# Kernel tuning notes

Measured on AMD Instinct MI355X. Metric: run time of the kernel, lower is better.

Reference implementation:

```python
import jax, jax.numpy as jnp
import numpy as np

N_NODES = 10000
N_EDGES = 640000
D_IN, D_HID, D_OUT = 128, 256, 64


def setup_inputs() -> dict:
    key = jax.random.key(0)
    k = jax.random.split(key, 8)
    h = jax.random.normal(k[0], (N_NODES, D_IN), dtype=jnp.float32)
    w = jax.random.uniform(k[1], (N_EDGES, 1), dtype=jnp.float32)
    src = jax.random.randint(k[2], (N_EDGES,), 0, N_NODES, dtype=jnp.int32)
    dst = jax.random.randint(k[3], (N_EDGES,), 0, N_NODES, dtype=jnp.int32)
    W1 = jax.random.normal(k[4], (2 * D_IN, D_HID), dtype=jnp.float32) * (1.0 / np.sqrt(2 * D_IN))
    b1 = jnp.zeros((D_HID,), dtype=jnp.float32)
    W2 = jax.random.normal(k[5], (2 * D_HID, D_OUT), dtype=jnp.float32) * (1.0 / np.sqrt(2 * D_HID))
    b2 = jnp.zeros((D_OUT,), dtype=jnp.float32)
    return {"h": h, "w": w, "src": src, "dst": dst, "W1": W1, "b1": b1, "W2": W2, "b2": b2}


def _sage_layer(h, w, src, dst, W, b, n_nodes):
    # message: m_e = h[src_e] * w_e  (scalar edge weight broadcast over features)
    m = h[src] * w  # [E, D]
    # mean scatter-reduce over incoming edges per destination node
    s = jax.ops.segment_sum(m, dst, num_segments=n_nodes)          # [N, D]
    deg = jax.ops.segment_sum(jnp.ones((dst.shape[0],), h.dtype), dst, num_segments=n_nodes)
    h_N = jnp.where(deg[:, None] > 0, s / jnp.maximum(deg, 1.0)[:, None], 0.0)
    # concat + linear
    return jnp.concatenate([h, h_N], axis=1) @ W + b


def reference(h, w, src, dst, W1, b1, W2, b2):
    n = h.shape[0]
    x = _sage_layer(h, w, src, dst, W1, b1, n)
    x = jax.nn.relu(x)
    return _sage_layer(x, w, src, dst, W2, b2, n)
```

## Files before the change

kernel.cpp:

```cpp
#include <hip/hip_runtime.h>
#include <hip/hip_fp16.h>


#define NSUB 4
#define CAPS 64
#define FB 2048

typedef _Float16 f16x8 __attribute__((ext_vector_type(8)));
typedef float f32x4 __attribute__((ext_vector_type(4)));

#define ACC8(q, wt)                                              \
  {                                                              \
    const float2 t0 = __half22float2(*(const __half2*)&(q).x);   \
    const float2 t1 = __half22float2(*(const __half2*)&(q).y);   \
    const float2 t2 = __half22float2(*(const __half2*)&(q).z);   \
    const float2 t3 = __half22float2(*(const __half2*)&(q).w);   \
    a[0] += t0.x * (wt); a[1] += t0.y * (wt);                    \
    a[2] += t1.x * (wt); a[3] += t1.y * (wt);                    \
    a[4] += t2.x * (wt); a[5] += t2.y * (wt);                    \
    a[6] += t3.x * (wt); a[7] += t3.y * (wt);                    \
  }


__global__ __launch_bounds__(256) void fill_k(const int* __restrict__ src,
                                              const int* __restrict__ dst,
                                              const float* __restrict__ w,
                                              const float* __restrict__ h,
                                              const float* __restrict__ W1,
                                              const float* __restrict__ W2,
                                              int* __restrict__ cursor,
                                              unsigned int* __restrict__ ebuf,
                                              __half* __restrict__ hh,
                                              __half* __restrict__ W1z,
                                              __half* __restrict__ W2z,
                                              int E, int N, int NH4) {
  if (blockIdx.x < FB) {
    const int grp = blockIdx.x & 7;
    const int bi = blockIdx.x >> 3;
    const int nbg = FB >> 3;
    const int chunk = (N + 7) >> 3;
    const int lo = grp * chunk;
    const int hi = min(N, lo + chunk);
    for (int i = bi * 256 + threadIdx.x; i < E; i += nbg * 256) {
      const int d = dst[i];
      if (d >= lo && d < hi) {
        const int sub = i & (NSUB - 1);
        const int p = atomicAdd(&cursor[d * NSUB + sub], 1);
        if (p < CAPS) {
          const __half hw = __float2half_rn(w[i]);
          ebuf[((size_t)(d * NSUB + sub)) * CAPS + p] =
              ((unsigned int)src[i] << 16) | (unsigned int)__half_as_ushort(hw);
        }
      }
    }
    return;
  }
  const int t = (blockIdx.x - FB) * 256 + threadIdx.x;
  if (t < NH4) {
    const float4 v = reinterpret_cast<const float4*>(h)[t];
    reinterpret_cast<__half2*>(hh)[2 * t] = __floats2half2_rn(v.x, v.y);
    reinterpret_cast<__half2*>(hh)[2 * t + 1] = __floats2half2_rn(v.z, v.w);
    return;
  }
  const int tw1 = t - NH4;
  if (tw1 < 8192) {
    const int ln = tw1 & 63;
    const int nt = (tw1 >> 6) & 15;
    const int kc = tw1 >> 10;
    const int kbase = kc * 32 + (ln >> 4) * 8;
    const int n = nt * 16 + (ln & 15);
    __half tmp[8];
#pragma unroll
    for (int j = 0; j < 8; ++j)
      tmp[j] = __float2half_rn(W1[(size_t)(kbase + j) * 256 + n]);
    *reinterpret_cast<uint4*>(W1z + (size_t)tw1 * 8) = *reinterpret_cast<uint4*>(tmp);
    return;
  }
  const int tw2 = tw1 - 8192;
  if (tw2 < 4096) {
    const int ln = tw2 & 63;
    const int nt = (tw2 >> 6) & 7;
    const int kc = tw2 >> 9;
    const int kbase = kc * 32 + (ln >> 4) * 8;
    const int np = nt * 16 + (ln & 15);
    __half tmp[8];
#pragma unroll
    for (int j = 0; j < 8; ++j) {
      const int k = kbase + j;
      const float v = (np < 64) ? W2[(size_t)k * 64 + np]
                                : W2[(size_t)(256 + k) * 64 + (np - 64)];
      tmp[j] = __float2half_rn(v);
    }
    *reinterpret_cast<uint4*>(W2z + (size_t)tw2 * 8) = *reinterpret_cast<uint4*>(tmp);
  }
}


__global__ __launch_bounds__(256) void ag1g_k(const __half* __restrict__ hh,
                                              const unsigned int* __restrict__ ebuf,
                                              const int* __restrict__ cnt,
                                              const __half* __restrict__ W1z,
                                              const float* __restrict__ b1,
                                              const __half* __restrict__ W2z,
                                              __half* __restrict__ Z,
                                              float* __restrict__ U, int N) {
  const int chunk = (N + 7) >> 3;
  const int g8 = blockIdx.x & 7;
  const int kb = blockIdx.x >> 3;
  const int locbase = kb * 16;
  const int nbase = g8 * chunk + locbase;
  const int tid = threadIdx.x;
  const int wv = tid >> 6;
  const int lane = tid & 63;
  const int g = lane >> 4;
  const int f = lane & 15;

  __shared__ alignas(16) __half As[16][136];
  __shared__ alignas(16) __half Hs[16][264];
  __shared__ alignas(16) float S[16][132];

  const uint4* __restrict__ H = reinterpret_cast<const uint4*>(hh);

#pragma unroll
  for (int i = 0; i < 4; ++i) {
    const int row = wv * 4 + i;
    const int loc = locbase + row;
    const int n = g8 * chunk + loc;
    const bool valid = (loc < chunk) && (n < N);
    int m[NSUB] = {0, 0, 0, 0};
    unsigned int pk[NSUB] = {0u, 0u, 0u, 0u};
    if (valid) {
      const int4 c4 = *reinterpret_cast<const int4*>(cnt + n * NSUB);
      m[0] = min(c4.x, CAPS);
      m[1] = min(c4.y, CAPS);
      m[2] = min(c4.z, CAPS);
      m[3] = min(c4.w, CAPS);
      const unsigned int* __restrict__ bkt = ebuf + ((size_t)(n * NSUB)) * CAPS;
#pragma unroll
      for (int s = 0; s < NSUB; ++s)
        pk[s] = (lane < m[s]) ? bkt[s * CAPS + lane] : 0u;
    }
    const int deg = m[0] + m[1] + m[2] + m[3];
    const int mMax = max(max(m[0], m[1]), max(m[2], m[3]));

    float a[8] = {};
    for (int j = 0; j < mMax; j += 4) {
      unsigned int p[NSUB];
#pragma unroll
      for (int s = 0; s < NSUB; ++s) p[s] = __shfl(pk[s], j + g);
      uint4 q[NSUB];
#pragma unroll
      for (int s = 0; s < NSUB; ++s) q[s] = H[(size_t)(p[s] >> 16) * 16 + f];
#pragma unroll
      for (int s = 0; s < NSUB; ++s) {
        const float wt = __half2float(__ushort_as_half((unsigned short)p[s]));
        ACC8(q[s], wt)
      }
    }
#pragma unroll
    for (int r = 0; r < 8; ++r) {
      a[r] += __shfl_xor(a[r], 16);
      a[r] += __shfl_xor(a[r], 32);
    }
    if (lane < 16) {
      const float inv = (deg > 0) ? 1.0f / (float)deg : 0.0f;
      __half tmp[8];
#pragma unroll
      for (int r = 0; r < 8; ++r) tmp[r] = __float2half_rn(a[r] * inv);
      *reinterpret_cast<uint4*>(&As[row][f * 8]) = *reinterpret_cast<uint4*>(tmp);
    }
  }
  __syncthreads();

  const int w = wv;
  const int row_in = nbase + (lane & 15);
  const int qoff = (lane >> 4) * 8;
  const int colq = lane & 15;
  const int rowq = (lane >> 4) * 4;

  f32x4 acc[4] = {};
  const __half* __restrict__ Ah = hh + (size_t)row_in * 128;
#pragma unroll
  for (int kc = 0; kc < 8; ++kc) {
    const __half* asrc =
        (kc < 4) ? (Ah + kc * 32 + qoff) : (&As[lane & 15][(kc - 4) * 32 + qoff]);
    const f16x8 af = *reinterpret_cast<const f16x8*>(asrc);
    const __half* bbase = W1z + ((size_t)(kc * 16 + w * 4) * 64 + lane) * 8;
#pragma unroll
    for (int nt = 0; nt < 4; ++nt) {
      const f16x8 bf = *reinterpret_cast<const f16x8*>(bbase + (size_t)nt * 64 * 8);
      acc[nt] = __builtin_amdgcn_mfma_f32_16x16x32_f16(af, bf, acc[nt], 0, 0, 0);
    }
  }
#pragma unroll
  for (int nt = 0; nt < 4; ++nt) {
    const int col = w * 64 + nt * 16 + colq;
    const float bz = b1[col];
#pragma unroll
    for (int r = 0; r < 4; ++r)
      Hs[rowq + r][col] = __float2half_rn(fmaxf(acc[nt][r] + bz, 0.f));
  }
  __syncthreads();

  f32x4 accz[2] = {};
#pragma unroll
  for (int kc = 0; kc < 8; ++kc) {
    const f16x8 af = *reinterpret_cast<const f16x8*>(&Hs[lane & 15][kc * 32 + qoff]);
    const __half* bbase = W2z + ((size_t)(kc * 8 + w * 2) * 64 + lane) * 8;
#pragma unroll
    for (int nt = 0; nt < 2; ++nt) {
      const f16x8 bf = *reinterpret_cast<const f16x8*>(bbase + (size_t)nt * 64 * 8);
      accz[nt] = __builtin_amdgcn_mfma_f32_16x16x32_f16(af, bf, accz[nt], 0, 0, 0);
    }
  }
#pragma unroll
  for (int nt = 0; nt < 2; ++nt) {
    const int col = w * 32 + nt * 16 + colq;
#pragma unroll
    for (int r = 0; r < 4; ++r) S[rowq + r][col] = accz[nt][r];
  }
  __syncthreads();
  {
    const int row = tid >> 4, c4 = tid & 15;
    if (locbase + row < chunk && nbase + row < N) {
      const float4 v = make_float4(S[row][c4 * 4], S[row][c4 * 4 + 1],
                                   S[row][c4 * 4 + 2], S[row][c4 * 4 + 3]);
      *reinterpret_cast<float4*>(&U[(size_t)(nbase + row) * 64 + c4 * 4]) = v;
    }
  }
  if (tid < 128) {
    const int row = tid >> 3, c8 = tid & 7;
    if (locbase + row < chunk && nbase + row < N) {
      const float* s = &S[row][64 + c8 * 8];
      const __half2 h0 = __floats2half2_rn(s[0], s[1]);
      const __half2 h1 = __floats2half2_rn(s[2], s[3]);
      const __half2 h2 = __floats2half2_rn(s[4], s[5]);
      const __half2 h3 = __floats2half2_rn(s[6], s[7]);
      uint4 q;
      q.x = *reinterpret_cast<const unsigned int*>(&h0);
      q.y = *reinterpret_cast<const unsigned int*>(&h1);
      q.z = *reinterpret_cast<const unsigned int*>(&h2);
      q.w = *reinterpret_cast<const unsigned int*>(&h3);
      *reinterpret_cast<uint4*>(&Z[(size_t)(nbase + row) * 64 + c8 * 8]) = q;
    }
  }
}


__global__ __launch_bounds__(256) void agg2z_k(const __half* __restrict__ Z,
                                               const float* __restrict__ U,
                                               const float* __restrict__ b2,
                                               const unsigned int* __restrict__ ebuf,
                                               const int* __restrict__ cnt,
                                               float* __restrict__ out, int N) {
  const int chunk = (N + 7) >> 3;
  const int g8 = blockIdx.x & 7;
  const int k = blockIdx.x >> 3;
  const int loc = k * 4 + (threadIdx.x >> 6);
  const int n = g8 * chunk + loc;
  if (loc >= chunk || n >= N) return;
  const int lane = threadIdx.x & 63;
  const int g = lane >> 3;
  const int f = lane & 7;
  const uint4* __restrict__ Zr = reinterpret_cast<const uint4*>(Z);

  const int4 c4 = *reinterpret_cast<const int4*>(cnt + n * NSUB);
  int m[NSUB];
  m[0] = min(c4.x, CAPS);
  m[1] = min(c4.y, CAPS);
  m[2] = min(c4.z, CAPS);
  m[3] = min(c4.w, CAPS);
  const int deg = m[0] + m[1] + m[2] + m[3];
  const int mMax = max(max(m[0], m[1]), max(m[2], m[3]));

  const unsigned int* __restrict__ bkt = ebuf + ((size_t)(n * NSUB)) * CAPS;
  unsigned int pk[NSUB];
#pragma unroll
  for (int s = 0; s < NSUB; ++s)
    pk[s] = (lane < m[s]) ? bkt[s * CAPS + lane] : 0u;

  float a[8] = {};
  for (int j = 0; j < mMax; j += 16) {
    unsigned int pA[NSUB], pB[NSUB];
#pragma unroll
    for (int s = 0; s < NSUB; ++s) {
      pA[s] = __shfl(pk[s], j + g);
      pB[s] = __shfl(pk[s], j + 8 + g);
    }
    uint4 qA[NSUB], qB[NSUB];
#pragma unroll
    for (int s = 0; s < NSUB; ++s) {
      qA[s] = Zr[(size_t)(pA[s] >> 16) * 8 + f];
      qB[s] = Zr[(size_t)(pB[s] >> 16) * 8 + f];
    }
#pragma unroll
    for (int s = 0; s < NSUB; ++s) {
      const float wA = __half2float(__ushort_as_half((unsigned short)pA[s]));
      const float wB = __half2float(__ushort_as_half((unsigned short)pB[s]));
      ACC8(qA[s], wA)
      ACC8(qB[s], wB)
    }
  }
#pragma unroll
  for (int r = 0; r < 8; ++r) {
    a[r] += __shfl_xor(a[r], 8);
    a[r] += __shfl_xor(a[r], 16);
    a[r] += __shfl_xor(a[r], 32);
  }
  if (lane < 8) {
    const float inv = (deg > 0) ? 1.0f / (float)deg : 0.0f;
    const float4 u0 = *reinterpret_cast<const float4*>(&U[(size_t)n * 64 + f * 8]);
    const float4 u1 = *reinterpret_cast<const float4*>(&U[(size_t)n * 64 + f * 8 + 4]);
    const float4 z0 = *reinterpret_cast<const float4*>(&b2[f * 8]);
    const float4 z1 = *reinterpret_cast<const float4*>(&b2[f * 8 + 4]);
    float4 o0, o1;
    o0.x = a[0] * inv + u0.x + z0.x;
    o0.y = a[1] * inv + u0.y + z0.y;
    o0.z = a[2] * inv + u0.z + z0.z;
    o0.w = a[3] * inv + u0.w + z0.w;
    o1.x = a[4] * inv + u1.x + z1.x;
    o1.y = a[5] * inv + u1.y + z1.y;
    o1.z = a[6] * inv + u1.z + z1.z;
    o1.w = a[7] * inv + u1.w + z1.w;
    *reinterpret_cast<float4*>(&out[(size_t)n * 64 + f * 8]) = o0;
    *reinterpret_cast<float4*>(&out[(size_t)n * 64 + f * 8 + 4]) = o1;
  }
}


extern "C" void kernel_launch(void* const* d_in, const int* in_sizes, int n_in,
                              void* d_out, int out_size, void* d_ws, size_t ws_size,
                              hipStream_t stream) {
  const float* h   = (const float*)d_in[0];
  const float* w   = (const float*)d_in[1];
  const int*   src = (const int*)d_in[2];
  const int*   dst = (const int*)d_in[3];
  const float* W1  = (const float*)d_in[4];
  const float* b1  = (const float*)d_in[5];
  const float* W2  = (const float*)d_in[6];
  const float* b2  = (const float*)d_in[7];
  float* out = (float*)d_out;

  const int N = in_sizes[0] / 128;
  const int E = in_sizes[2];

  char* ws = (char*)d_ws;
  size_t o = 0;
  auto alloc = [&](size_t bytes) -> void* {
    void* p = ws + o;
    o = (o + bytes + 255) & ~(size_t)255;
    return p;
  };
  int*          cursor = (int*)alloc((size_t)N * NSUB * 4);
  unsigned int* ebuf   = (unsigned int*)alloc((size_t)N * NSUB * CAPS * 4);
  __half*       hh     = (__half*)alloc((size_t)N * 128 * 2);
  __half*       Z      = (__half*)alloc((size_t)N * 64 * 2);
  float*        U      = (float*)alloc((size_t)N * 64 * 4);
  __half*       W1z    = (__half*)alloc((size_t)256 * 256 * 2);
  __half*       W2z    = (__half*)alloc((size_t)256 * 128 * 2);

  const int NH4 = N * 32;
  const int prep_blocks = (NH4 + 8192 + 4096 + 255) / 256;
  const int chunk = (N + 7) >> 3;

  hipMemsetAsync(cursor, 0, (size_t)N * NSUB * 4, stream);
  fill_k<<<FB + prep_blocks, 256, 0, stream>>>(src, dst, w, h, W1, W2, cursor,
                                               ebuf, hh, W1z, W2z, E, N, NH4);
  ag1g_k<<<8 * ((chunk + 15) >> 4), 256, 0, stream>>>(hh, ebuf, cursor, W1z, b1,
                                                      W2z, Z, U, N);
  agg2z_k<<<8 * ((chunk + 3) / 4), 256, 0, stream>>>(Z, U, b2, ebuf, cursor, out, N);
}
```

Before: 137.9 us.

## Interleave edge buckets and overlap four-row gathers in fused SAGE layer

Edge buckets are now stored interleaved by sub-bucket, so each lane loads its four packed entries with a single 16-byte load instead of four strided loads. The layer-1 aggregation processes a wave's four destination rows in one interleaved loop, which gives more independent gathers in flight and better latency hiding. It also prefetches the self-feature MFMA operands, biases and the layer-2 residual inputs ahead of the gather loop. The cost is higher register pressure from four accumulator sets, which may reduce occupancy.

```diff
diff --git a/kernel.cpp b/kernel.cpp
--- a/kernel.cpp
+++ b/kernel.cpp
@@ -9,16 +9,16 @@
 typedef _Float16 f16x8 __attribute__((ext_vector_type(8)));
 typedef float f32x4 __attribute__((ext_vector_type(4)));
 
-#define ACC8(q, wt)                                              \
+#define ACC8P(acc, q, wt)                                        \
   {                                                              \
     const float2 t0 = __half22float2(*(const __half2*)&(q).x);   \
     const float2 t1 = __half22float2(*(const __half2*)&(q).y);   \
     const float2 t2 = __half22float2(*(const __half2*)&(q).z);   \
     const float2 t3 = __half22float2(*(const __half2*)&(q).w);   \
-    a[0] += t0.x * (wt); a[1] += t0.y * (wt);                    \
-    a[2] += t1.x * (wt); a[3] += t1.y * (wt);                    \
-    a[4] += t2.x * (wt); a[5] += t2.y * (wt);                    \
-    a[6] += t3.x * (wt); a[7] += t3.y * (wt);                    \
+    (acc)[0] += t0.x * (wt); (acc)[1] += t0.y * (wt);            \
+    (acc)[2] += t1.x * (wt); (acc)[3] += t1.y * (wt);            \
+    (acc)[4] += t2.x * (wt); (acc)[5] += t2.y * (wt);            \
+    (acc)[6] += t3.x * (wt); (acc)[7] += t3.y * (wt);            \
   }
 
 
@@ -48,7 +48,7 @@
         const int p = atomicAdd(&cursor[d * NSUB + sub], 1);
         if (p < CAPS) {
           const __half hw = __float2half_rn(w[i]);
-          ebuf[((size_t)(d * NSUB + sub)) * CAPS + p] =
+          ebuf[((size_t)d * CAPS + p) * NSUB + sub] =
               ((unsigned int)src[i] << 16) | (unsigned int)__half_as_ushort(hw);
         }
       }
@@ -121,70 +121,91 @@
 
   const uint4* __restrict__ H = reinterpret_cast<const uint4*>(hh);
 
-#pragma unroll
-  for (int i = 0; i < 4; ++i) {
-    const int row = wv * 4 + i;
-    const int loc = locbase + row;
-    const int n = g8 * chunk + loc;
-    const bool valid = (loc < chunk) && (n < N);
-    int m[NSUB] = {0, 0, 0, 0};
-    unsigned int pk[NSUB] = {0u, 0u, 0u, 0u};
-    if (valid) {
-      const int4 c4 = *reinterpret_cast<const int4*>(cnt + n * NSUB);
-      m[0] = min(c4.x, CAPS);
-      m[1] = min(c4.y, CAPS);
-      m[2] = min(c4.z, CAPS);
-      m[3] = min(c4.w, CAPS);
-      const unsigned int* __restrict__ bkt = ebuf + ((size_t)(n * NSUB)) * CAPS;
-#pragma unroll
-      for (int s = 0; s < NSUB; ++s)
-        pk[s] = (lane < m[s]) ? bkt[s * CAPS + lane] : 0u;
-    }
-    const int deg = m[0] + m[1] + m[2] + m[3];
-    const int mMax = max(max(m[0], m[1]), max(m[2], m[3]));
-
-    float a[8] = {};
-    for (int j = 0; j < mMax; j += 4) {
-      unsigned int p[NSUB];
-#pragma unroll
-      for (int s = 0; s < NSUB; ++s) p[s] = __shfl(pk[s], j + g);
-      uint4 q[NSUB];
-#pragma unroll
-      for (int s = 0; s < NSUB; ++s) q[s] = H[(size_t)(p[s] >> 16) * 16 + f];
-#pragma unroll
-      for (int s = 0; s < NSUB; ++s) {
-        const float wt = __half2float(__ushort_as_half((unsigned short)p[s]));
-        ACC8(q[s], wt)
-      }
-    }
-#pragma unroll
-    for (int r = 0; r < 8; ++r) {
-      a[r] += __shfl_xor(a[r], 16);
-      a[r] += __shfl_xor(a[r], 32);
-    }
-    if (lane < 16) {
-      const float inv = (deg > 0) ? 1.0f / (float)deg : 0.0f;
-      __half tmp[8];
-#pragma unroll
-      for (int r = 0; r < 8; ++r) tmp[r] = __float2half_rn(a[r] * inv);
-      *reinterpret_cast<uint4*>(&As[row][f * 8]) = *reinterpret_cast<uint4*>(tmp);
-    }
-  }
-  __syncthreads();
-
-  const int w = wv;
   const int row_in = nbase + (lane & 15);
   const int qoff = (lane >> 4) * 8;
   const int colq = lane & 15;
   const int rowq = (lane >> 4) * 4;
-
+  const __half* __restrict__ Ah = hh + (size_t)row_in * 128;
+  f16x8 afp[4];
+#pragma unroll
+  for (int kc = 0; kc < 4; ++kc)
+    afp[kc] = *reinterpret_cast<const f16x8*>(Ah + kc * 32 + qoff);
+  float bz[4];
+#pragma unroll
+  for (int nt = 0; nt < 4; ++nt) bz[nt] = b1[wv * 64 + nt * 16 + colq];
+
+  int mM[4], degv[4];
+  unsigned int pk[4][NSUB];
+  float a[4][8];
+#pragma unroll
+  for (int i = 0; i < 4; ++i) {
+#pragma unroll
+    for (int r = 0; r < 8; ++r) a[i][r] = 0.f;
+    const int loc = locbase + wv * 4 + i;
+    const int n = g8 * chunk + loc;
+    const bool valid = (loc < chunk) && (n < N);
+    int m0 = 0, m1 = 0, m2 = 0, m3 = 0;
+    uint4 pkv = make_uint4(0u, 0u, 0u, 0u);
+    if (valid) {
+      const int4 c4 = *reinterpret_cast<const int4*>(cnt + n * NSUB);
+      m0 = min(c4.x, CAPS);
+      m1 = min(c4.y, CAPS);
+      m2 = min(c4.z, CAPS);
+      m3 = min(c4.w, CAPS);
+      pkv = *reinterpret_cast<const uint4*>(ebuf + ((size_t)n * CAPS + lane) * NSUB);
+    }
+    pk[i][0] = (lane < m0) ? pkv.x : 0u;
+    pk[i][1] = (lane < m1) ? pkv.y : 0u;
+    pk[i][2] = (lane < m2) ? pkv.z : 0u;
+    pk[i][3] = (lane < m3) ? pkv.w : 0u;
+    degv[i] = m0 + m1 + m2 + m3;
+    mM[i] = max(max(m0, m1), max(m2, m3));
+  }
+  const int maxAll = max(max(mM[0], mM[1]), max(mM[2], mM[3]));
+
+  for (int j = 0; j < maxAll; j += 4) {
+#pragma unroll
+    for (int i = 0; i < 4; ++i) {
+      if (j < mM[i]) {
+        unsigned int p[NSUB];
+#pragma unroll
+        for (int s = 0; s < NSUB; ++s) p[s] = __shfl(pk[i][s], j + g);
+        uint4 q[NSUB];
+#pragma unroll
+        for (int s = 0; s < NSUB; ++s) q[s] = H[(size_t)(p[s] >> 16) * 16 + f];
+#pragma unroll
+        for (int s = 0; s < NSUB; ++s) {
+          const float wt = __half2float(__ushort_as_half((unsigned short)p[s]));
+          ACC8P(a[i], q[s], wt)
+        }
+      }
+    }
+  }
+#pragma unroll
+  for (int i = 0; i < 4; ++i) {
+#pragma unroll
+    for (int r = 0; r < 8; ++r) {
+      a[i][r] += __shfl_xor(a[i][r], 16);
+      a[i][r] += __shfl_xor(a[i][r], 32);
+    }
+    if (lane < 16) {
+      const float inv = (degv[i] > 0) ? 1.0f / (float)degv[i] : 0.0f;
+      __half tmp[8];
+#pragma unroll
+      for (int r = 0; r < 8; ++r) tmp[r] = __float2half_rn(a[i][r] * inv);
+      *reinterpret_cast<uint4*>(&As[wv * 4 + i][f * 8]) =
+          *reinterpret_cast<uint4*>(tmp);
+    }
+  }
+  __syncthreads();
+
+  const int w = wv;
   f32x4 acc[4] = {};
-  const __half* __restrict__ Ah = hh + (size_t)row_in * 128;
 #pragma unroll
   for (int kc = 0; kc < 8; ++kc) {
-    const __half* asrc =
-        (kc < 4) ? (Ah + kc * 32 + qoff) : (&As[lane & 15][(kc - 4) * 32 + qoff]);
-    const f16x8 af = *reinterpret_cast<const f16x8*>(asrc);
+    const f16x8 af =
+        (kc < 4) ? afp[kc]
+                 : *reinterpret_cast<const f16x8*>(&As[lane & 15][(kc - 4) * 32 + qoff]);
     const __half* bbase = W1z + ((size_t)(kc * 16 + w * 4) * 64 + lane) * 8;
 #pragma unroll
     for (int nt = 0; nt < 4; ++nt) {
@@ -195,10 +216,9 @@
 #pragma unroll
   for (int nt = 0; nt < 4; ++nt) {
     const int col = w * 64 + nt * 16 + colq;
-    const float bz = b1[col];
 #pragma unroll
     for (int r = 0; r < 4; ++r)
-      Hs[rowq + r][col] = __float2half_rn(fmaxf(acc[nt][r] + bz, 0.f));
+      Hs[rowq + r][col] = __float2half_rn(fmaxf(acc[nt][r] + bz[nt], 0.f));
   }
   __syncthreads();
 
@@ -273,11 +293,18 @@
   const int deg = m[0] + m[1] + m[2] + m[3];
   const int mMax = max(max(m[0], m[1]), max(m[2], m[3]));
 
-  const unsigned int* __restrict__ bkt = ebuf + ((size_t)(n * NSUB)) * CAPS;
+  const uint4 pkv =
+      *reinterpret_cast<const uint4*>(ebuf + ((size_t)n * CAPS + lane) * NSUB);
   unsigned int pk[NSUB];
-#pragma unroll
-  for (int s = 0; s < NSUB; ++s)
-    pk[s] = (lane < m[s]) ? bkt[s * CAPS + lane] : 0u;
+  pk[0] = (lane < m[0]) ? pkv.x : 0u;
+  pk[1] = (lane < m[1]) ? pkv.y : 0u;
+  pk[2] = (lane < m[2]) ? pkv.z : 0u;
+  pk[3] = (lane < m[3]) ? pkv.w : 0u;
+
+  const float4 u0 = *reinterpret_cast<const float4*>(&U[(size_t)n * 64 + f * 8]);
+  const float4 u1 = *reinterpret_cast<const float4*>(&U[(size_t)n * 64 + f * 8 + 4]);
+  const float4 z0 = *reinterpret_cast<const float4*>(&b2[f * 8]);
+  const float4 z1 = *reinterpret_cast<const float4*>(&b2[f * 8 + 4]);
 
   float a[8] = {};
   for (int j = 0; j < mMax; j += 16) {
@@ -297,8 +324,8 @@
     for (int s = 0; s < NSUB; ++s) {
       const float wA = __half2float(__ushort_as_half((unsigned short)pA[s]));
       const float wB = __half2float(__ushort_as_half((unsigned short)pB[s]));
-      ACC8(qA[s], wA)
-      ACC8(qB[s], wB)
+      ACC8P(a, qA[s], wA)
+      ACC8P(a, qB[s], wB)
     }
   }
 #pragma unroll
@@ -309,10 +336,6 @@
   }
   if (lane < 8) {
     const float inv = (deg > 0) ? 1.0f / (float)deg : 0.0f;
-    const float4 u0 = *reinterpret_cast<const float4*>(&U[(size_t)n * 64 + f * 8]);
-    const float4 u1 = *reinterpret_cast<const float4*>(&U[(size_t)n * 64 + f * 8 + 4]);
-    const float4 z0 = *reinterpret_cast<const float4*>(&b2[f * 8]);
-    const float4 z1 = *reinterpret_cast<const float4*>(&b2[f * 8 + 4]);
     float4 o0, o1;
     o0.x = a[0] * inv + u0.x + z0.x;
     o0.y = a[1] * inv + u0.y + z0.y;
```

Result: no change. 138.0 us, median of 2 (+0.1%).
